# Kernel optimization log

Measured on AMD Instinct MI355X. Metric: run time of the kernel, lower is better.

The kernel has to match this reference:

```python
import jax, jax.numpy as jnp
import numpy as np

TANH_CONST = 2.5
TEMPERATURE = 5.0


def setup_inputs() -> dict:
    key = jax.random.key(0)
    ks = jax.random.split(key, 9)
    B, L, NB, H, NC = 16384, 64, 8, 128, 1000
    return {
        "class_ids": jax.random.randint(ks[0], (B,), 0, NC),
        "gumbel_u": jax.random.uniform(ks[1], (L, B, NB), dtype=jnp.float32),
        "g_emb": jax.random.normal(ks[2], (NC, H), dtype=jnp.float32) * 0.1,
        "w_emb": jax.random.normal(ks[3], (NB, H), dtype=jnp.float32) * 0.1,
        "w_soft": jax.random.normal(ks[4], (NB, H), dtype=jnp.float32) * 0.1,
        "w_ih": jax.random.normal(ks[5], (4 * H, H), dtype=jnp.float32) * 0.1,
        "w_hh": jax.random.normal(ks[6], (4 * H, H), dtype=jnp.float32) * 0.1,
        "b_ih": jax.random.normal(ks[7], (4 * H,), dtype=jnp.float32) * 0.1,
        "b_hh": jax.random.normal(ks[8], (4 * H,), dtype=jnp.float32) * 0.1,
    }


def reference(class_ids, gumbel_u, g_emb, w_emb, w_soft, w_ih, w_hh, b_ih, b_hh):
    B = class_ids.shape[0]
    H = g_emb.shape[1]
    x0 = g_emb[class_ids]                      # [B, H] class embedding (reused each step)
    h0 = jnp.zeros((B, H), x0.dtype)
    c0 = jnp.zeros((B, H), x0.dtype)

    def step(carry, u):
        h, c, x = carry
        gates = x @ w_ih.T + h @ w_hh.T + b_ih + b_hh   # [B, 4H], torch gate order i,f,g,o
        i, f, g, o = jnp.split(gates, 4, axis=-1)
        c2 = jax.nn.sigmoid(f) * c + jax.nn.sigmoid(i) * jnp.tanh(g)
        h2 = jax.nn.sigmoid(o) * jnp.tanh(c2)
        logit = h2 @ w_soft.T                           # [B, NB]
        logit = TANH_CONST * jnp.tanh(logit / TEMPERATURE)
        # categorical sample via gumbel-max
        uc = jnp.clip(u, 1e-8, 1.0 - 1e-8)
        gmb = -jnp.log(-jnp.log(uc))
        branch = jnp.argmax(logit + gmb, axis=-1)       # [B] int
        logp = jax.nn.log_softmax(logit, axis=-1)
        lp = jnp.take_along_axis(logp, branch[:, None], axis=1)[:, 0]
        ent = -jnp.sum(jnp.exp(logp) * logp, axis=-1)
        x2 = (w_emb[branch] + x0) * 0.5
        return (h2, c2, x2), (branch, lp, ent)

    _, (arcs, lps, ents) = jax.lax.scan(step, (h0, c0, x0), gumbel_u)
    # stack along dim=1 like torch.stack(..., dim=1) -> [B, L]
    sample_arc = arcs.T
    sample_log_prob = lps.T
    sample_entropy = ents.T
    sample_prob = jnp.exp(sample_log_prob)
    return sample_arc, sample_log_prob, sample_entropy, sample_prob
```

## Files before the change

### kernel.cpp

```cpp
#include <hip/hip_runtime.h>
#include <math.h>

#define HD 128
#define NBR 8
#define LSTEPS 64
#define TILE_B 32
#define HT_PAD 36
#define PART_PAD 132

#define WPT_OFF   0
#define WIPT_OFF  65536
#define PP_OFF    131072
#define BSUM_OFF  135168

__global__ __launch_bounds__(256) void setup_kernel(
    const float* __restrict__ w_emb, const float* __restrict__ w_ih,
    const float* __restrict__ w_hh, const float* __restrict__ b_ih,
    const float* __restrict__ b_hh, float* __restrict__ ws)
{
  int tid = blockIdx.x * blockDim.x + threadIdx.x;
  if (tid < 65536) {
    int k = tid >> 9, col = tid & 511;
    int hh = col >> 2, q = col & 3;
    ws[WPT_OFF + tid]  = w_hh[(q*HD + hh)*HD + k];
    ws[WIPT_OFF + tid] = w_ih[(q*HD + hh)*HD + k];
  }
  if (tid < 4096) {
    int j = tid >> 9, rem = tid & 511;
    int q = rem >> 7, hh2 = rem & 127;
    const float* wr = w_ih + (q*HD + hh2)*HD;
    const float* er = w_emb + j*HD;
    float s = 0.f;
    for (int k = 0; k < HD; ++k) s = fmaf(er[k], wr[k], s);
    ws[PP_OFF + (size_t)j*512 + 4*hh2 + q] = s + b_ih[q*HD + hh2] + b_hh[q*HD + hh2];
  }
  if (tid < 512) {
    int q = tid >> 7, hh2 = tid & 127;
    ws[BSUM_OFF + tid] = b_ih[q*HD + hh2] + b_hh[q*HD + hh2];
  }
}

__device__ __forceinline__ float fsig(float x) {
  return __fdividef(1.f, 1.f + __expf(-x));
}
__device__ __forceinline__ float ftanh(float x) {
  float ax = fabsf(x);
  float e  = __expf(-2.f * ax);
  float r  = __fdividef(1.f - e, 1.f + e);
  return copysignf(r, x);
}

#define ROWQ(qi, wq) \
  acc[qi][0] = fmaf(ha.x, wq, acc[qi][0]); acc[qi][1] = fmaf(ha.y, wq, acc[qi][1]); \
  acc[qi][2] = fmaf(ha.z, wq, acc[qi][2]); acc[qi][3] = fmaf(ha.w, wq, acc[qi][3]); \
  acc[qi][4] = fmaf(hb.x, wq, acc[qi][4]); acc[qi][5] = fmaf(hb.y, wq, acc[qi][5]); \
  acc[qi][6] = fmaf(hb.z, wq, acc[qi][6]); acc[qi][7] = fmaf(hb.w, wq, acc[qi][7]);

#define KSTEP(WPTR, HPTR) do { \
    float4 w  = *(const float4*)(WPTR); \
    float4 ha = *(const float4*)(HPTR); \
    float4 hb = *(const float4*)((HPTR) + 4); \
    ROWQ(0, w.x) ROWQ(1, w.y) ROWQ(2, w.z) ROWQ(3, w.w) \
  } while (0)

__global__ __launch_bounds__(512, 4) void ctrl_kernel(
    const int* __restrict__ class_ids,
    const float* __restrict__ gumbel_u,
    const float* __restrict__ g_emb,
    const float* __restrict__ w_soft,
    const float* __restrict__ ws,
    float* __restrict__ out,
    int Btot)
{
  __shared__ __align__(16) float hT0[HD * HT_PAD];
  __shared__ __align__(16) float hT1[HD * HT_PAD];
  __shared__ __align__(16) float wsoft_l[NBR * HD];
  __shared__ __align__(16) float part_l[TILE_B * PART_PAD];
  __shared__ __align__(16) float pp_l[NBR * 512];
  __shared__ int br_l[TILE_B];

  const int tid = threadIdx.x;
  const int b0  = blockIdx.x * TILE_B;
  const size_t BL = (size_t)Btot * LSTEPS;

  const float* __restrict__ wpT  = ws + WPT_OFF;
  const float* __restrict__ wipT = ws + WIPT_OFF;

  for (int i = tid; i < NBR*HD; i += 512) wsoft_l[i] = w_soft[i];
  for (int i = tid; i < NBR*512; i += 512) pp_l[i] = ws[PP_OFF + i];

  const int hh = tid & 127;
  const int bg = tid >> 7;

  {
    int sb = tid >> 4;
    int kc = tid & 15;
    int cid = class_ids[b0 + sb];
    const float* src = g_emb + (size_t)cid * HD + kc*8;
    float4 v0 = *(const float4*)(src);
    float4 v1 = *(const float4*)(src + 4);
    int kb = kc*8;
    hT0[(kb+0)*HT_PAD + sb] = v0.x;
    hT0[(kb+1)*HT_PAD + sb] = v0.y;
    hT0[(kb+2)*HT_PAD + sb] = v0.z;
    hT0[(kb+3)*HT_PAD + sb] = v0.w;
    hT0[(kb+4)*HT_PAD + sb] = v1.x;
    hT0[(kb+5)*HT_PAD + sb] = v1.y;
    hT0[(kb+6)*HT_PAD + sb] = v1.z;
    hT0[(kb+7)*HT_PAD + sb] = v1.w;
  }
  __syncthreads();

  float qpark[32];
  {
    float acc[4][8];
    #pragma unroll
    for (int q = 0; q < 4; ++q)
      #pragma unroll
      for (int j = 0; j < 8; ++j) acc[q][j] = 0.f;

    const float* wrow = wipT + 4*hh;
    const float* hr   = hT0 + bg*8;
    #pragma unroll 2
    for (int k = 0; k < HD; ++k) {
      KSTEP(wrow, hr);
      wrow += 512; hr += HT_PAD;
    }
    #pragma unroll
    for (int q = 0; q < 4; ++q) {
      float bs = ws[BSUM_OFF + q*HD + hh];
      #pragma unroll
      for (int j = 0; j < 8; ++j) {
        float v = 0.5f * (acc[q][j] + bs);
        asm("v_accvgpr_write_b32 %0, %1" : "=a"(qpark[q*8+j]) : "v"(v));
      }
    }
  }
  __syncthreads();

  float c[8];
  #pragma unroll
  for (int j = 0; j < 8; ++j) c[j] = 0.f;

  float* hcur = hT0;
  float* hnxt = hT1;

  for (int t = 0; t < LSTEPS; ++t) {
    float gmb[8];
    if (tid < TILE_B) {
      const float* up = gumbel_u + ((size_t)t * Btot + (b0 + tid)) * NBR;
      float4 ua = *(const float4*)up;
      float4 ub = *(const float4*)(up + 4);
      float uv[8] = {ua.x,ua.y,ua.z,ua.w,ub.x,ub.y,ub.z,ub.w};
      #pragma unroll
      for (int nb = 0; nb < 8; ++nb) {
        float uc = fminf(fmaxf(uv[nb], 1e-8f), 0.99999999f);
        gmb[nb] = -__logf(-__logf(uc));
      }
    }

    float acc[4][8];
    #pragma unroll
    for (int q = 0; q < 4; ++q)
      #pragma unroll
      for (int j = 0; j < 8; ++j)
        asm("v_accvgpr_read_b32 %0, %1" : "=v"(acc[q][j]) : "a"(qpark[q*8+j]));

    if (t > 0) {
      __builtin_amdgcn_s_setprio(1);
      const float* wrow = wpT + 4*hh;
      const float* hr   = hcur + bg*8;
      #pragma unroll 2
      for (int k = 0; k < HD; ++k) {
        KSTEP(wrow, hr);
        wrow += 512; hr += HT_PAD;
      }
      __builtin_amdgcn_s_setprio(0);
    }

    float h2v[8];
    #pragma unroll
    for (int j = 0; j < 8; ++j) {
      float gi, gf, gg, go;
      if (t == 0) {
        gi = 2.f*acc[0][j]; gf = 2.f*acc[1][j];
        gg = 2.f*acc[2][j]; go = 2.f*acc[3][j];
      } else {
        int br = br_l[bg*8 + j];
        float4 pv = *(const float4*)(&pp_l[br*512 + 4*hh]);
        gi = fmaf(0.5f, pv.x, acc[0][j]);
        gf = fmaf(0.5f, pv.y, acc[1][j]);
        gg = fmaf(0.5f, pv.z, acc[2][j]);
        go = fmaf(0.5f, pv.w, acc[3][j]);
      }
      float iv = fsig(gi);
      float fv = fsig(gf);
      float gv = ftanh(gg);
      float ov = fsig(go);
      float c2 = fmaf(fv, c[j], iv*gv);
      c[j] = c2;
      h2v[j] = ov * ftanh(c2);
    }

    {
      float* dst = &hnxt[hh*HT_PAD + bg*8];
      *(float4*)(dst)   = make_float4(h2v[0],h2v[1],h2v[2],h2v[3]);
      *(float4*)(dst+4) = make_float4(h2v[4],h2v[5],h2v[6],h2v[7]);
    }
    __syncthreads();

    {
      int lb = tid & 31, ch = tid >> 5;
      const float* hp = hnxt + (ch*8)*HT_PAD + lb;
      float hv[8];
      #pragma unroll
      for (int i = 0; i < 8; ++i) hv[i] = hp[i*HT_PAD];
      #pragma unroll
      for (int nb = 0; nb < 8; ++nb) {
        const float4* wr = (const float4*)&wsoft_l[nb*HD + ch*8];
        float4 wa = wr[0], wb = wr[1];
        float p = 0.f;
        p = fmaf(hv[0], wa.x, p); p = fmaf(hv[1], wa.y, p);
        p = fmaf(hv[2], wa.z, p); p = fmaf(hv[3], wa.w, p);
        p = fmaf(hv[4], wb.x, p); p = fmaf(hv[5], wb.y, p);
        p = fmaf(hv[6], wb.z, p); p = fmaf(hv[7], wb.w, p);
        part_l[lb*PART_PAD + nb*16 + ch] = p;
      }
    }
    __syncthreads();

    if (tid < TILE_B) {
      int lb = tid;
      float lg[8];
      #pragma unroll
      for (int nb = 0; nb < 8; ++nb) {
        const float4* pr = (const float4*)&part_l[lb*PART_PAD + nb*16];
        float4 pa = pr[0], pb = pr[1], pc = pr[2], pd = pr[3];
        float s = pa.x; s += pa.y; s += pa.z; s += pa.w;
        s += pb.x; s += pb.y; s += pb.z; s += pb.w;
        s += pc.x; s += pc.y; s += pc.z; s += pc.w;
        s += pd.x; s += pd.y; s += pd.z; s += pd.w;
        lg[nb] = 2.5f * ftanh(s * 0.2f);
      }
      int br = 0; float best = lg[0] + gmb[0];
      #pragma unroll
      for (int nb = 1; nb < 8; ++nb) {
        float y = lg[nb] + gmb[nb];
        if (y > best) { best = y; br = nb; }
      }
      br_l[lb] = br;
      float m = lg[0];
      #pragma unroll
      for (int nb = 1; nb < 8; ++nb) m = fmaxf(m, lg[nb]);
      float se = 0.f;
      #pragma unroll
      for (int nb = 0; nb < 8; ++nb) se += __expf(lg[nb] - m);
      float lse = __logf(se);
      float lp = (lg[br] - m) - lse;
      size_t row = (size_t)(b0 + lb) * LSTEPS + t;
      out[row]        = (float)br;
      out[BL + row]   = lp;
      out[3*BL + row] = __expf(lp);
      float ent = 0.f;
      #pragma unroll
      for (int nb = 0; nb < 8; ++nb) {
        float lpi = (lg[nb] - m) - lse;
        ent -= __expf(lpi) * lpi;
      }
      out[2*BL + row] = ent;
    }
    __syncthreads();

    float* tmp = hcur; hcur = hnxt; hnxt = tmp;
  }
}

extern "C" void kernel_launch(void* const* d_in, const int* in_sizes, int n_in,
                              void* d_out, int out_size, void* d_ws, size_t ws_size,
                              hipStream_t stream) {
  const int*   class_ids = (const int*)d_in[0];
  const float* gumbel_u  = (const float*)d_in[1];
  const float* g_emb     = (const float*)d_in[2];
  const float* w_emb     = (const float*)d_in[3];
  const float* w_soft    = (const float*)d_in[4];
  const float* w_ih      = (const float*)d_in[5];
  const float* w_hh      = (const float*)d_in[6];
  const float* b_ih      = (const float*)d_in[7];
  const float* b_hh      = (const float*)d_in[8];
  float* out = (float*)d_out;
  float* ws  = (float*)d_ws;
  int B = in_sizes[0];

  hipLaunchKernelGGL(setup_kernel, dim3(256), dim3(256), 0, stream,
                     w_emb, w_ih, w_hh, b_ih, b_hh, ws);
  hipLaunchKernelGGL(ctrl_kernel, dim3(B / TILE_B), dim3(512), 0, stream,
                     class_ids, gumbel_u, g_emb, w_soft, ws, out, B);
}
```

Baseline: 2.080 ms.

## Software-pipeline recurrent matvec loads and parallelize logit reduction with shuffles

The h@W_hh inner loop now double-buffers its LDS reads, loading weights and hidden values for step k+2 while FMAs run on step k. The per-sample logit reduction and sampling, previously done by 32 threads serially summing 16 partials each, is spread across 512 threads and finished with xor-shuffles inside 16-lane groups. __syncthreads is replaced with a barrier that waits only on lgkmcnt, skipping the wait on outstanding global stores. Prefetching needs more registers, which could limit occupancy. Dropping the vmcnt wait relies on global stores being independent of the shared-memory handoff.

```diff
diff --git a/kernel.cpp b/kernel.cpp
--- a/kernel.cpp
+++ b/kernel.cpp
@@ -50,18 +50,16 @@
   return copysignf(r, x);
 }
 
-#define ROWQ(qi, wq) \
-  acc[qi][0] = fmaf(ha.x, wq, acc[qi][0]); acc[qi][1] = fmaf(ha.y, wq, acc[qi][1]); \
-  acc[qi][2] = fmaf(ha.z, wq, acc[qi][2]); acc[qi][3] = fmaf(ha.w, wq, acc[qi][3]); \
-  acc[qi][4] = fmaf(hb.x, wq, acc[qi][4]); acc[qi][5] = fmaf(hb.y, wq, acc[qi][5]); \
-  acc[qi][6] = fmaf(hb.z, wq, acc[qi][6]); acc[qi][7] = fmaf(hb.w, wq, acc[qi][7]);
-
-#define KSTEP(WPTR, HPTR) do { \
-    float4 w  = *(const float4*)(WPTR); \
-    float4 ha = *(const float4*)(HPTR); \
-    float4 hb = *(const float4*)((HPTR) + 4); \
-    ROWQ(0, w.x) ROWQ(1, w.y) ROWQ(2, w.z) ROWQ(3, w.w) \
-  } while (0)
+#define ROWQ(qi, wq, HA, HB) \
+  acc[qi][0] = fmaf((HA).x, wq, acc[qi][0]); acc[qi][1] = fmaf((HA).y, wq, acc[qi][1]); \
+  acc[qi][2] = fmaf((HA).z, wq, acc[qi][2]); acc[qi][3] = fmaf((HA).w, wq, acc[qi][3]); \
+  acc[qi][4] = fmaf((HB).x, wq, acc[qi][4]); acc[qi][5] = fmaf((HB).y, wq, acc[qi][5]); \
+  acc[qi][6] = fmaf((HB).z, wq, acc[qi][6]); acc[qi][7] = fmaf((HB).w, wq, acc[qi][7]);
+
+#define KFMA(W, HA, HB) \
+  ROWQ(0, (W).x, HA, HB) ROWQ(1, (W).y, HA, HB) ROWQ(2, (W).z, HA, HB) ROWQ(3, (W).w, HA, HB)
+
+#define BAR_LGKM() asm volatile("s_waitcnt lgkmcnt(0)\n\ts_barrier" ::: "memory")
 
 __global__ __launch_bounds__(512, 4) void ctrl_kernel(
     const int* __restrict__ class_ids,
@@ -91,6 +89,8 @@
 
   const int hh = tid & 127;
   const int bg = tid >> 7;
+  const int slb = tid >> 4;
+  const int sr  = tid & 15;
 
   {
     int sb = tid >> 4;
@@ -119,12 +119,15 @@
       #pragma unroll
       for (int j = 0; j < 8; ++j) acc[q][j] = 0.f;
 
-    const float* wrow = wipT + 4*hh;
-    const float* hr   = hT0 + bg*8;
+    const float* wr = wipT + 4*hh;
+    const float* hr = hT0 + bg*8;
     #pragma unroll 2
     for (int k = 0; k < HD; ++k) {
-      KSTEP(wrow, hr);
-      wrow += 512; hr += HT_PAD;
+      float4 w  = *(const float4*)(wr);
+      float4 ha = *(const float4*)(hr);
+      float4 hb = *(const float4*)(hr + 4);
+      KFMA(w, ha, hb);
+      wr += 512; hr += HT_PAD;
     }
     #pragma unroll
     for (int q = 0; q < 4; ++q) {
@@ -147,8 +150,8 @@
 
   for (int t = 0; t < LSTEPS; ++t) {
     float gmb[8];
-    if (tid < TILE_B) {
-      const float* up = gumbel_u + ((size_t)t * Btot + (b0 + tid)) * NBR;
+    if (sr == 0) {
+      const float* up = gumbel_u + ((size_t)t * Btot + (b0 + slb)) * NBR;
       float4 ua = *(const float4*)up;
       float4 ub = *(const float4*)(up + 4);
       float uv[8] = {ua.x,ua.y,ua.z,ua.w,ub.x,ub.y,ub.z,ub.w};
@@ -168,13 +171,30 @@
 
     if (t > 0) {
       __builtin_amdgcn_s_setprio(1);
-      const float* wrow = wpT + 4*hh;
-      const float* hr   = hcur + bg*8;
-      #pragma unroll 2
-      for (int k = 0; k < HD; ++k) {
-        KSTEP(wrow, hr);
-        wrow += 512; hr += HT_PAD;
-      }
+      const float* wr = wpT + 4*hh;
+      const float* hr = hcur + bg*8;
+      float4 w0 = *(const float4*)(wr);
+      float4 w1 = *(const float4*)(wr + 512);
+      float4 a0 = *(const float4*)(hr);
+      float4 b0v = *(const float4*)(hr + 4);
+      float4 a1 = *(const float4*)(hr + HT_PAD);
+      float4 b1 = *(const float4*)(hr + HT_PAD + 4);
+      #pragma unroll 3
+      for (int kb = 0; kb < 63; ++kb) {
+        float4 wc = w0, ac = a0, bc = b0v;
+        w0  = *(const float4*)(wr + 2*512);
+        a0  = *(const float4*)(hr + 2*HT_PAD);
+        b0v = *(const float4*)(hr + 2*HT_PAD + 4);
+        KFMA(wc, ac, bc);
+        float4 wd = w1, ad = a1, bd = b1;
+        w1 = *(const float4*)(wr + 3*512);
+        a1 = *(const float4*)(hr + 3*HT_PAD);
+        b1 = *(const float4*)(hr + 3*HT_PAD + 4);
+        KFMA(wd, ad, bd);
+        wr += 1024; hr += 2*HT_PAD;
+      }
+      KFMA(w0, a0, b0v);
+      KFMA(w1, a1, b1);
       __builtin_amdgcn_s_setprio(0);
     }
 
@@ -207,7 +227,7 @@
       *(float4*)(dst)   = make_float4(h2v[0],h2v[1],h2v[2],h2v[3]);
       *(float4*)(dst+4) = make_float4(h2v[4],h2v[5],h2v[6],h2v[7]);
     }
-    __syncthreads();
+    BAR_LGKM();
 
     {
       int lb = tid & 31, ch = tid >> 5;
@@ -217,8 +237,8 @@
       for (int i = 0; i < 8; ++i) hv[i] = hp[i*HT_PAD];
       #pragma unroll
       for (int nb = 0; nb < 8; ++nb) {
-        const float4* wr = (const float4*)&wsoft_l[nb*HD + ch*8];
-        float4 wa = wr[0], wb = wr[1];
+        const float4* wr2 = (const float4*)&wsoft_l[nb*HD + ch*8];
+        float4 wa = wr2[0], wb = wr2[1];
         float p = 0.f;
         p = fmaf(hv[0], wa.x, p); p = fmaf(hv[1], wa.y, p);
         p = fmaf(hv[2], wa.z, p); p = fmaf(hv[3], wa.w, p);
@@ -227,49 +247,53 @@
         part_l[lb*PART_PAD + nb*16 + ch] = p;
       }
     }
-    __syncthreads();
-
-    if (tid < TILE_B) {
-      int lb = tid;
-      float lg[8];
-      #pragma unroll
-      for (int nb = 0; nb < 8; ++nb) {
-        const float4* pr = (const float4*)&part_l[lb*PART_PAD + nb*16];
-        float4 pa = pr[0], pb = pr[1], pc = pr[2], pd = pr[3];
-        float s = pa.x; s += pa.y; s += pa.z; s += pa.w;
-        s += pb.x; s += pb.y; s += pb.z; s += pb.w;
-        s += pc.x; s += pc.y; s += pc.z; s += pc.w;
-        s += pd.x; s += pd.y; s += pd.z; s += pd.w;
-        lg[nb] = 2.5f * ftanh(s * 0.2f);
-      }
-      int br = 0; float best = lg[0] + gmb[0];
-      #pragma unroll
-      for (int nb = 1; nb < 8; ++nb) {
-        float y = lg[nb] + gmb[nb];
-        if (y > best) { best = y; br = nb; }
-      }
-      br_l[lb] = br;
-      float m = lg[0];
-      #pragma unroll
-      for (int nb = 1; nb < 8; ++nb) m = fmaxf(m, lg[nb]);
-      float se = 0.f;
-      #pragma unroll
-      for (int nb = 0; nb < 8; ++nb) se += __expf(lg[nb] - m);
-      float lse = __logf(se);
-      float lp = (lg[br] - m) - lse;
-      size_t row = (size_t)(b0 + lb) * LSTEPS + t;
-      out[row]        = (float)br;
-      out[BL + row]   = lp;
-      out[3*BL + row] = __expf(lp);
-      float ent = 0.f;
-      #pragma unroll
-      for (int nb = 0; nb < 8; ++nb) {
-        float lpi = (lg[nb] - m) - lse;
-        ent -= __expf(lpi) * lpi;
-      }
-      out[2*BL + row] = ent;
-    }
-    __syncthreads();
+    BAR_LGKM();
+
+    {
+      float s[8];
+      #pragma unroll
+      for (int nb = 0; nb < 8; ++nb)
+        s[nb] = part_l[slb*PART_PAD + nb*16 + sr];
+      #pragma unroll
+      for (int mk = 1; mk < 16; mk <<= 1) {
+        #pragma unroll
+        for (int nb = 0; nb < 8; ++nb)
+          s[nb] += __shfl_xor(s[nb], mk, 64);
+      }
+      if (sr == 0) {
+        float lg[8];
+        #pragma unroll
+        for (int nb = 0; nb < 8; ++nb)
+          lg[nb] = 2.5f * ftanh(s[nb] * 0.2f);
+        int br = 0; float best = lg[0] + gmb[0];
+        #pragma unroll
+        for (int nb = 1; nb < 8; ++nb) {
+          float y = lg[nb] + gmb[nb];
+          if (y > best) { best = y; br = nb; }
+        }
+        br_l[slb] = br;
+        float m = lg[0];
+        #pragma unroll
+        for (int nb = 1; nb < 8; ++nb) m = fmaxf(m, lg[nb]);
+        float se = 0.f;
+        #pragma unroll
+        for (int nb = 0; nb < 8; ++nb) se += __expf(lg[nb] - m);
+        float lse = __logf(se);
+        float lp = (lg[br] - m) - lse;
+        float ent = 0.f;
+        #pragma unroll
+        for (int nb = 0; nb < 8; ++nb) {
+          float lpi = (lg[nb] - m) - lse;
+          ent -= __expf(lpi) * lpi;
+        }
+        size_t row = (size_t)(b0 + slb) * LSTEPS + t;
+        out[row]        = (float)br;
+        out[BL + row]   = lp;
+        out[2*BL + row] = ent;
+        out[3*BL + row] = __expf(lp);
+      }
+    }
+    BAR_LGKM();
 
     float* tmp = hcur; hcur = hnxt; hnxt = tmp;
   }
```

New measurement: 2.282 ms. 9.7% more time.
